# Kernel tuning notes

Measured on AMD Instinct MI355X. Metric: run time of the kernel, lower is better.

Reference implementation:

```python
import jax, jax.numpy as jnp
import numpy as np

D_MODEL = 2048
NUM_EXPERTS = 64
TOP_K = 2


def setup_inputs() -> dict:
    key = jax.random.key(0)
    k_x, k_w = jax.random.split(key)
    x = jax.random.normal(k_x, (4, 8192, D_MODEL), dtype=jnp.float32)
    # nn.Linear(d_model, num_experts, bias=False): weight [num_experts, d_model]
    bound = 1.0 / np.sqrt(D_MODEL)
    W = jax.random.uniform(k_w, (NUM_EXPERTS, D_MODEL), dtype=jnp.float32,
                           minval=-bound, maxval=bound)
    return {"x": x, "W": W}


def reference(x, W):
    # router_logits = x @ W.T : [b, s, num_experts]
    logits = jnp.einsum("bsd,ed->bse", x, W)
    probs = jax.nn.softmax(logits, axis=-1)
    gates, indices = jax.lax.top_k(probs, TOP_K)  # [b, s, top_k]
    gates = gates / jnp.sum(gates, axis=-1, keepdims=True)
    return gates, indices
```

## Files before the change

### kernel.cpp

```cpp
#include <hip/hip_runtime.h>
#include <math.h>
#include <stdint.h>

#define D_MODEL 2048
#define NEXP    64
#define TOKENS  32768
#define BM      64
#define BK      64
#define NT      256
#define NCHUNK  (D_MODEL / BK)
#define TIE_THR 1e-3f
#define LSTRIDE 66

typedef __attribute__((ext_vector_type(8))) short short8;
typedef __attribute__((ext_vector_type(4))) float f32x4;
typedef __attribute__((ext_vector_type(4))) int   i32x4;

typedef __attribute__((address_space(3))) uint32_t       lds_u32_t;
typedef const __attribute__((address_space(1))) uint32_t gbl_u32_t;

#define STAGE(c, b)                                                            \
    _Pragma("unroll")                                                          \
    for (int g = 0; g < 4; ++g) {                                              \
        const int G_ = 4 * wave + g;                                           \
        __builtin_amdgcn_global_load_lds((gbl_u32_t*)(xsrc[g] + (size_t)(c) * BK), \
                                         (lds_u32_t*)&xs[b][4 * G_][0], 16, 0, 0); \
        __builtin_amdgcn_global_load_lds((gbl_u32_t*)(wsrc[g] + (size_t)(c) * BK), \
                                         (lds_u32_t*)&ws[b][4 * G_][0], 16, 0, 0); \
    }

__device__ __forceinline__ void split2(float f0, float f1, uint32_t& hw, uint32_t& lw)
{
    const uint32_t u0 = __float_as_uint(f0), u1 = __float_as_uint(f1);
    const uint32_t a0 = u0 & 0xffff0000u,  a1 = u1 & 0xffff0000u;
    hw = a1 | (u0 >> 16);
    const float l0 = f0 - __uint_as_float(a0);
    const float l1 = f1 - __uint_as_float(a1);
    lw = (__float_as_uint(l1) & 0xffff0000u) | (__float_as_uint(l0) >> 16);
}

__device__ __forceinline__ void ldsplit(const char* p0, const char* p1,
                                        short8& h8, short8& l8)
{
    const float4 qa = *(const float4*)p0;
    const float4 qb = *(const float4*)p1;
    i32x4 hv, lv;
    uint32_t hw, lw;
    split2(qa.x, qa.y, hw, lw); hv[0] = (int)hw; lv[0] = (int)lw;
    split2(qa.z, qa.w, hw, lw); hv[1] = (int)hw; lv[1] = (int)lw;
    split2(qb.x, qb.y, hw, lw); hv[2] = (int)hw; lv[2] = (int)lw;
    split2(qb.z, qb.w, hw, lw); hv[3] = (int)hw; lv[3] = (int)lw;
    h8 = *(short8*)&hv;
    l8 = *(short8*)&lv;
}

__global__ __launch_bounds__(NT, 2)
void router_kernel(const float* __restrict__ x, const float* __restrict__ W,
                   float* __restrict__ out)
{
    __shared__ float xs[2][BM][BK];
    __shared__ float ws[2][NEXP][BK];
    __shared__ int   flaglist[BM];
    __shared__ int   nflag;

    const int tid  = threadIdx.x;
    const int lane = tid & 63;
    const int wave = tid >> 6;
    const int row0 = blockIdx.x * BM;

    const int lrow  = lane >> 4;
    const int lslot = lane & 15;
    const float* xsrc[4];
    const float* wsrc[4];
#pragma unroll
    for (int g = 0; g < 4; ++g) {
        const int r   = 16 * wave + 4 * g + lrow;
        const int col = 4 * (lslot ^ (r & 7));
        xsrc[g] = x + (size_t)(row0 + r) * D_MODEL + col;
        wsrc[g] = W + (size_t)r * D_MODEL + col;
    }

    const int fr  = lane & 15;
    const int h   = lane >> 4;
    const int sw  = 16 * (fr & 7);
    const int t0b = (32 * h) ^ sw;
    const int mt0 = 2 * (wave & 1);
    const int nt0 = 2 * (wave >> 1);
    const int rowA[2] = { (16 * (mt0 + 0) + fr) * 256, (16 * (mt0 + 1) + fr) * 256 };
    const int rowB[2] = { (16 * (nt0 + 0) + fr) * 256, (16 * (nt0 + 1) + fr) * 256 };

    f32x4 acc[2][2] = {};

    STAGE(0, 0);
    __syncthreads();

    for (int c = 0; c < NCHUNK; ++c) {
        const int buf = c & 1;
        if (c + 1 < NCHUNK) STAGE(c + 1, buf ^ 1);
        const char* xb = (const char*)&xs[buf][0][0];
        const char* wb = (const char*)&ws[buf][0][0];
#pragma unroll
        for (int s = 0; s < 2; ++s) {
            const int off0 = 128 * s + t0b;
            short8 ah[2], al[2], bh[2], bl[2];
#pragma unroll
            for (int mi = 0; mi < 2; ++mi)
                ldsplit(xb + rowA[mi] + off0, xb + rowA[mi] + (off0 ^ 16), ah[mi], al[mi]);
#pragma unroll
            for (int ni = 0; ni < 2; ++ni)
                ldsplit(wb + rowB[ni] + off0, wb + rowB[ni] + (off0 ^ 16), bh[ni], bl[ni]);
#pragma unroll
            for (int mi = 0; mi < 2; ++mi)
#pragma unroll
                for (int ni = 0; ni < 2; ++ni) {
                    acc[mi][ni] = __builtin_amdgcn_mfma_f32_16x16x32_bf16(ah[mi], bh[ni], acc[mi][ni], 0, 0, 0);
                    acc[mi][ni] = __builtin_amdgcn_mfma_f32_16x16x32_bf16(al[mi], bh[ni], acc[mi][ni], 0, 0, 0);
                    acc[mi][ni] = __builtin_amdgcn_mfma_f32_16x16x32_bf16(ah[mi], bl[ni], acc[mi][ni], 0, 0, 0);
                }
        }
        __syncthreads();
    }

    float* logits = (float*)&xs[0][0][0];
#pragma unroll
    for (int mi = 0; mi < 2; ++mi)
#pragma unroll
        for (int ni = 0; ni < 2; ++ni)
#pragma unroll
            for (int r = 0; r < 4; ++r)
                logits[(16 * (mt0 + mi) + 4 * h + r) * LSTRIDE + 16 * (nt0 + ni) + fr] =
                    acc[mi][ni][r];
    if (tid == 0) nflag = 0;
    __syncthreads();

    float m1 = -INFINITY, m2 = -INFINITY, m3 = -INFINITY;
    int   i1 = 0, i2 = 0;
    bool  tie = false;
    if (tid < BM) {
#pragma unroll 8
        for (int e = 0; e < NEXP; ++e) {
            const float v = logits[tid * LSTRIDE + e];
            if (v > m1)      { m3 = m2; m2 = m1; i2 = i1; m1 = v; i1 = e; }
            else if (v > m2) { m3 = m2; m2 = v; i2 = e; }
            else if (v > m3) { m3 = v; }
        }
        tie = (m1 - m2 < TIE_THR) || (m2 - m3 < TIE_THR);
        if (tie) { const int p = atomicAdd(&nflag, 1); flaglist[p] = tid; }
    }
    __syncthreads();

    const int nf = nflag;
    float* partial = (float*)&ws[0][0][0];
    for (int f = 0; f < nf; ++f) {
        const int t = flaglist[f];
        const float* xr   = x + (size_t)(row0 + t) * D_MODEL + 512 * wave;
        const float* wrow = W + (size_t)lane * D_MODEL + 512 * wave;
        float ps = 0.f;
        for (int k = 0; k < 512; k += 4) {
            const float4 xv = *(const float4*)(xr + k);
            const float4 wv = *(const float4*)(wrow + k);
            ps = fmaf(xv.x, wv.x, ps); ps = fmaf(xv.y, wv.y, ps);
            ps = fmaf(xv.z, wv.z, ps); ps = fmaf(xv.w, wv.w, ps);
        }
        partial[wave * 64 + lane] = ps;
        __syncthreads();
        if (tid < NEXP)
            logits[t * LSTRIDE + tid] = (partial[tid] + partial[64 + tid]) +
                                        (partial[128 + tid] + partial[192 + tid]);
        __syncthreads();
    }

    if (tid < BM) {
        if (tie) {
            m1 = -INFINITY; m2 = -INFINITY; i1 = 0; i2 = 0;
#pragma unroll 8
            for (int e = 0; e < NEXP; ++e) {
                const float v = logits[tid * LSTRIDE + e];
                if (v > m1)      { m2 = m1; i2 = i1; m1 = v; i1 = e; }
                else if (v > m2) { m2 = v; i2 = e; }
            }
        }
        const float ex = expf(m2 - m1);
        const float g1 = 1.0f / (1.0f + ex);
        const float g2 = ex * g1;
        const int row = row0 + tid;
        out[(size_t)row * 2 + 0] = g1;
        out[(size_t)row * 2 + 1] = g2;
        out[(size_t)TOKENS * 2 + (size_t)row * 2 + 0] = (float)i1;
        out[(size_t)TOKENS * 2 + (size_t)row * 2 + 1] = (float)i2;
    }
}

extern "C" void kernel_launch(void* const* d_in, const int* in_sizes, int n_in,
                              void* d_out, int out_size, void* d_ws, size_t ws_size,
                              hipStream_t stream) {
    const float* x = (const float*)d_in[0];
    const float* W = (const float*)d_in[1];
    float* out = (float*)d_out;
    router_kernel<<<TOKENS / BM, NT, 0, stream>>>(x, W, out);
}
```

Before: 179.0 us.

## Use 128-row tiles, 8 waves, and a 4-stage async LDS pipeline

After: 183.6 us. 2.6% more time.

```diff
diff --git a/kernel.cpp b/kernel.cpp
--- a/kernel.cpp
+++ b/kernel.cpp
@@ -5,10 +5,11 @@
 #define D_MODEL 2048
 #define NEXP    64
 #define TOKENS  32768
-#define BM      64
-#define BK      64
-#define NT      256
+#define BM      128
+#define BK      32
+#define NT      512
 #define NCHUNK  (D_MODEL / BK)
+#define BUFSZ   24576
 #define TIE_THR 1e-3f
 #define LSTRIDE 66
 
@@ -19,20 +20,10 @@
 typedef __attribute__((address_space(3))) uint32_t       lds_u32_t;
 typedef const __attribute__((address_space(1))) uint32_t gbl_u32_t;
 
-#define STAGE(c, b)                                                            \
-    _Pragma("unroll")                                                          \
-    for (int g = 0; g < 4; ++g) {                                              \
-        const int G_ = 4 * wave + g;                                           \
-        __builtin_amdgcn_global_load_lds((gbl_u32_t*)(xsrc[g] + (size_t)(c) * BK), \
-                                         (lds_u32_t*)&xs[b][4 * G_][0], 16, 0, 0); \
-        __builtin_amdgcn_global_load_lds((gbl_u32_t*)(wsrc[g] + (size_t)(c) * BK), \
-                                         (lds_u32_t*)&ws[b][4 * G_][0], 16, 0, 0); \
-    }
-
 __device__ __forceinline__ void split2(float f0, float f1, uint32_t& hw, uint32_t& lw)
 {
     const uint32_t u0 = __float_as_uint(f0), u1 = __float_as_uint(f1);
-    const uint32_t a0 = u0 & 0xffff0000u,  a1 = u1 & 0xffff0000u;
+    const uint32_t a0 = u0 & 0xffff0000u, a1 = u1 & 0xffff0000u;
     hw = a1 | (u0 >> 16);
     const float l0 = f0 - __uint_as_float(a0);
     const float l1 = f1 - __uint_as_float(a1);
@@ -54,81 +45,99 @@
     l8 = *(short8*)&lv;
 }
 
+#define WAITVM(N) asm volatile("s_waitcnt vmcnt(" #N ")" ::: "memory")
+
+#define STAGE(c, b)                                                              \
+    do {                                                                         \
+        char* bb_ = smem + (b) * BUFSZ;                                          \
+        __builtin_amdgcn_global_load_lds((gbl_u32_t*)(xsrc0 + (size_t)(c) * BK), \
+            (lds_u32_t*)(bb_ + 2048 * wave), 16, 0, 0);                          \
+        __builtin_amdgcn_global_load_lds((gbl_u32_t*)(xsrc1 + (size_t)(c) * BK), \
+            (lds_u32_t*)(bb_ + 2048 * wave + 1024), 16, 0, 0);                   \
+        __builtin_amdgcn_global_load_lds((gbl_u32_t*)(wsrc0 + (size_t)(c) * BK), \
+            (lds_u32_t*)(bb_ + 16384 + 1024 * wave), 16, 0, 0);                  \
+    } while (0)
+
+#define COMPUTE(b)                                                               \
+    do {                                                                         \
+        const char* xb_ = smem + (b) * BUFSZ;                                    \
+        const char* wb_ = xb_ + 16384;                                           \
+        short8 ah_[2], al_[2], bh_[2], bl_[2];                                   \
+        _Pragma("unroll")                                                        \
+        for (int mi = 0; mi < 2; ++mi)                                           \
+            ldsplit(xb_ + oA[mi], xb_ + (oA[mi] ^ 16), ah_[mi], al_[mi]);        \
+        _Pragma("unroll")                                                        \
+        for (int ni = 0; ni < 2; ++ni)                                           \
+            ldsplit(wb_ + oB[ni], wb_ + (oB[ni] ^ 16), bh_[ni], bl_[ni]);        \
+        _Pragma("unroll")                                                        \
+        for (int mi = 0; mi < 2; ++mi)                                           \
+            _Pragma("unroll")                                                    \
+            for (int ni = 0; ni < 2; ++ni) {                                     \
+                acc[mi][ni] = __builtin_amdgcn_mfma_f32_16x16x32_bf16(ah_[mi], bh_[ni], acc[mi][ni], 0, 0, 0); \
+                acc[mi][ni] = __builtin_amdgcn_mfma_f32_16x16x32_bf16(al_[mi], bh_[ni], acc[mi][ni], 0, 0, 0); \
+                acc[mi][ni] = __builtin_amdgcn_mfma_f32_16x16x32_bf16(ah_[mi], bl_[ni], acc[mi][ni], 0, 0, 0); \
+            }                                                                    \
+    } while (0)
+
 __global__ __launch_bounds__(NT, 2)
 void router_kernel(const float* __restrict__ x, const float* __restrict__ W,
                    float* __restrict__ out)
 {
-    __shared__ float xs[2][BM][BK];
-    __shared__ float ws[2][NEXP][BK];
-    __shared__ int   flaglist[BM];
-    __shared__ int   nflag;
+    __shared__ char smem[4 * BUFSZ];
+    __shared__ int  flaglist[BM];
+    __shared__ int  nflag;
 
     const int tid  = threadIdx.x;
     const int lane = tid & 63;
     const int wave = tid >> 6;
     const int row0 = blockIdx.x * BM;
 
-    const int lrow  = lane >> 4;
-    const int lslot = lane & 15;
-    const float* xsrc[4];
-    const float* wsrc[4];
-#pragma unroll
-    for (int g = 0; g < 4; ++g) {
-        const int r   = 16 * wave + 4 * g + lrow;
-        const int col = 4 * (lslot ^ (r & 7));
-        xsrc[g] = x + (size_t)(row0 + r) * D_MODEL + col;
-        wsrc[g] = W + (size_t)r * D_MODEL + col;
-    }
-
-    const int fr  = lane & 15;
-    const int h   = lane >> 4;
-    const int sw  = 16 * (fr & 7);
-    const int t0b = (32 * h) ^ sw;
-    const int mt0 = 2 * (wave & 1);
-    const int nt0 = 2 * (wave >> 1);
-    const int rowA[2] = { (16 * (mt0 + 0) + fr) * 256, (16 * (mt0 + 1) + fr) * 256 };
-    const int rowB[2] = { (16 * (nt0 + 0) + fr) * 256, (16 * (nt0 + 1) + fr) * 256 };
+    const int srow = lane >> 3;
+    const int scol = 4 * ((lane & 7) ^ srow);
+    const float* xsrc0 = x + (size_t)(row0 + 16 * wave + srow) * D_MODEL + scol;
+    const float* xsrc1 = x + (size_t)(row0 + 16 * wave + 8 + srow) * D_MODEL + scol;
+    const float* wsrc0 = W + (size_t)(8 * wave + srow) * D_MODEL + scol;
+
+    const int fr = lane & 15;
+    const int h  = lane >> 4;
+    const int m0 = 32 * (wave >> 1);
+    const int n0 = 32 * (wave & 1);
+    int oA[2], oB[2];
+#pragma unroll
+    for (int i = 0; i < 2; ++i) {
+        oA[i] = (m0 + 16 * i + fr) * 128 + 16 * ((2 * h) ^ (fr & 7));
+        oB[i] = (n0 + 16 * i + fr) * 128 + 16 * ((2 * h) ^ (fr & 7));
+    }
 
     f32x4 acc[2][2] = {};
 
     STAGE(0, 0);
+    STAGE(1, 1);
+    STAGE(2, 2);
+
+    for (int c = 0; c < NCHUNK - 3; ++c) {
+        WAITVM(6);
+        __builtin_amdgcn_s_barrier();
+        __builtin_amdgcn_sched_barrier(0);
+        STAGE(c + 3, (c + 3) & 3);
+        COMPUTE(c & 3);
+    }
+    WAITVM(6); __builtin_amdgcn_s_barrier(); __builtin_amdgcn_sched_barrier(0);
+    COMPUTE((NCHUNK - 3) & 3);
+    WAITVM(3); __builtin_amdgcn_s_barrier(); __builtin_amdgcn_sched_barrier(0);
+    COMPUTE((NCHUNK - 2) & 3);
+    WAITVM(0); __builtin_amdgcn_s_barrier(); __builtin_amdgcn_sched_barrier(0);
+    COMPUTE((NCHUNK - 1) & 3);
     __syncthreads();
 
-    for (int c = 0; c < NCHUNK; ++c) {
-        const int buf = c & 1;
-        if (c + 1 < NCHUNK) STAGE(c + 1, buf ^ 1);
-        const char* xb = (const char*)&xs[buf][0][0];
-        const char* wb = (const char*)&ws[buf][0][0];
-#pragma unroll
-        for (int s = 0; s < 2; ++s) {
-            const int off0 = 128 * s + t0b;
-            short8 ah[2], al[2], bh[2], bl[2];
-#pragma unroll
-            for (int mi = 0; mi < 2; ++mi)
-                ldsplit(xb + rowA[mi] + off0, xb + rowA[mi] + (off0 ^ 16), ah[mi], al[mi]);
-#pragma unroll
-            for (int ni = 0; ni < 2; ++ni)
-                ldsplit(wb + rowB[ni] + off0, wb + rowB[ni] + (off0 ^ 16), bh[ni], bl[ni]);
-#pragma unroll
-            for (int mi = 0; mi < 2; ++mi)
-#pragma unroll
-                for (int ni = 0; ni < 2; ++ni) {
-                    acc[mi][ni] = __builtin_amdgcn_mfma_f32_16x16x32_bf16(ah[mi], bh[ni], acc[mi][ni], 0, 0, 0);
-                    acc[mi][ni] = __builtin_amdgcn_mfma_f32_16x16x32_bf16(al[mi], bh[ni], acc[mi][ni], 0, 0, 0);
-                    acc[mi][ni] = __builtin_amdgcn_mfma_f32_16x16x32_bf16(ah[mi], bl[ni], acc[mi][ni], 0, 0, 0);
-                }
-        }
-        __syncthreads();
-    }
-
-    float* logits = (float*)&xs[0][0][0];
+    float* logits = (float*)smem;
 #pragma unroll
     for (int mi = 0; mi < 2; ++mi)
 #pragma unroll
         for (int ni = 0; ni < 2; ++ni)
 #pragma unroll
             for (int r = 0; r < 4; ++r)
-                logits[(16 * (mt0 + mi) + 4 * h + r) * LSTRIDE + 16 * (nt0 + ni) + fr] =
+                logits[(m0 + 16 * mi + 4 * h + r) * LSTRIDE + n0 + 16 * ni + fr] =
                     acc[mi][ni][r];
     if (tid == 0) nflag = 0;
     __syncthreads();
@@ -150,13 +159,13 @@
     __syncthreads();
 
     const int nf = nflag;
-    float* partial = (float*)&ws[0][0][0];
+    float* partial = (float*)(smem + 65536);
     for (int f = 0; f < nf; ++f) {
         const int t = flaglist[f];
-        const float* xr   = x + (size_t)(row0 + t) * D_MODEL + 512 * wave;
-        const float* wrow = W + (size_t)lane * D_MODEL + 512 * wave;
+        const float* xr   = x + (size_t)(row0 + t) * D_MODEL + 256 * wave;
+        const float* wrow = W + (size_t)lane * D_MODEL + 256 * wave;
         float ps = 0.f;
-        for (int k = 0; k < 512; k += 4) {
+        for (int k = 0; k < 256; k += 4) {
             const float4 xv = *(const float4*)(xr + k);
             const float4 wv = *(const float4*)(wrow + k);
             ps = fmaf(xv.x, wv.x, ps); ps = fmaf(xv.y, wv.y, ps);
@@ -164,9 +173,12 @@
         }
         partial[wave * 64 + lane] = ps;
         __syncthreads();
-        if (tid < NEXP)
-            logits[t * LSTRIDE + tid] = (partial[tid] + partial[64 + tid]) +
-                                        (partial[128 + tid] + partial[192 + tid]);
+        if (tid < NEXP) {
+            float s = 0.f;
+#pragma unroll
+            for (int wv = 0; wv < 8; ++wv) s += partial[wv * 64 + tid];
+            logits[t * LSTRIDE + tid] = s;
+        }
         __syncthreads();
     }
 
```

## Load GEMM operands directly from global into registers, drop LDS staging

Applied to the files above, without the earlier changes.

Result: slower. 267.5 us (+49.4%).

```diff
diff --git a/kernel.cpp b/kernel.cpp
--- a/kernel.cpp
+++ b/kernel.cpp
@@ -6,9 +6,8 @@
 #define NEXP    64
 #define TOKENS  32768
 #define BM      64
-#define BK      64
 #define NT      256
-#define NCHUNK  (D_MODEL / BK)
+#define NCHUNK  (D_MODEL / 32)
 #define TIE_THR 1e-3f
 #define LSTRIDE 66
 
@@ -16,34 +15,19 @@
 typedef __attribute__((ext_vector_type(4))) float f32x4;
 typedef __attribute__((ext_vector_type(4))) int   i32x4;
 
-typedef __attribute__((address_space(3))) uint32_t       lds_u32_t;
-typedef const __attribute__((address_space(1))) uint32_t gbl_u32_t;
-
-#define STAGE(c, b)                                                            \
-    _Pragma("unroll")                                                          \
-    for (int g = 0; g < 4; ++g) {                                              \
-        const int G_ = 4 * wave + g;                                           \
-        __builtin_amdgcn_global_load_lds((gbl_u32_t*)(xsrc[g] + (size_t)(c) * BK), \
-                                         (lds_u32_t*)&xs[b][4 * G_][0], 16, 0, 0); \
-        __builtin_amdgcn_global_load_lds((gbl_u32_t*)(wsrc[g] + (size_t)(c) * BK), \
-                                         (lds_u32_t*)&ws[b][4 * G_][0], 16, 0, 0); \
-    }
-
 __device__ __forceinline__ void split2(float f0, float f1, uint32_t& hw, uint32_t& lw)
 {
     const uint32_t u0 = __float_as_uint(f0), u1 = __float_as_uint(f1);
-    const uint32_t a0 = u0 & 0xffff0000u,  a1 = u1 & 0xffff0000u;
+    const uint32_t a0 = u0 & 0xffff0000u, a1 = u1 & 0xffff0000u;
     hw = a1 | (u0 >> 16);
     const float l0 = f0 - __uint_as_float(a0);
     const float l1 = f1 - __uint_as_float(a1);
     lw = (__float_as_uint(l1) & 0xffff0000u) | (__float_as_uint(l0) >> 16);
 }
 
-__device__ __forceinline__ void ldsplit(const char* p0, const char* p1,
-                                        short8& h8, short8& l8)
+__device__ __forceinline__ void regsplit(const float4 qa, const float4 qb,
+                                         short8& h8, short8& l8)
 {
-    const float4 qa = *(const float4*)p0;
-    const float4 qb = *(const float4*)p1;
     i32x4 hv, lv;
     uint32_t hw, lw;
     split2(qa.x, qa.y, hw, lw); hv[0] = (int)hw; lv[0] = (int)lw;
@@ -54,12 +38,32 @@
     l8 = *(short8*)&lv;
 }
 
+#define ASTEP(c, CA0, CA1, NA0, NA1, DOPREF)                                   \
+    do {                                                                       \
+        if (DOPREF) {                                                          \
+            NA0 = *(const float4*)(xrow + 32 * ((c) + 1));                     \
+            NA1 = *(const float4*)(xrow + 32 * ((c) + 1) + 4);                 \
+        }                                                                      \
+        short8 ah_, al_;                                                       \
+        regsplit(CA0, CA1, ah_, al_);                                          \
+        _Pragma("unroll")                                                      \
+        for (int n = 0; n < 4; ++n) {                                          \
+            const float4 qb0 = *(const float4*)(wrow[n] + 32 * (c));           \
+            const float4 qb1 = *(const float4*)(wrow[n] + 32 * (c) + 4);       \
+            short8 bh_, bl_;                                                   \
+            regsplit(qb0, qb1, bh_, bl_);                                      \
+            acc[n] = __builtin_amdgcn_mfma_f32_16x16x32_bf16(ah_, bh_, acc[n], 0, 0, 0); \
+            acc[n] = __builtin_amdgcn_mfma_f32_16x16x32_bf16(al_, bh_, acc[n], 0, 0, 0); \
+            acc[n] = __builtin_amdgcn_mfma_f32_16x16x32_bf16(ah_, bl_, acc[n], 0, 0, 0); \
+        }                                                                      \
+    } while (0)
+
 __global__ __launch_bounds__(NT, 2)
 void router_kernel(const float* __restrict__ x, const float* __restrict__ W,
                    float* __restrict__ out)
 {
-    __shared__ float xs[2][BM][BK];
-    __shared__ float ws[2][NEXP][BK];
+    __shared__ float logits[BM * LSTRIDE];
+    __shared__ float partial[4 * 64];
     __shared__ int   flaglist[BM];
     __shared__ int   nflag;
 
@@ -68,68 +72,30 @@
     const int wave = tid >> 6;
     const int row0 = blockIdx.x * BM;
 
-    const int lrow  = lane >> 4;
-    const int lslot = lane & 15;
-    const float* xsrc[4];
-    const float* wsrc[4];
+    const int fr = lane & 15;
+    const int h  = lane >> 4;
+    const float* xrow = x + (size_t)(row0 + 16 * wave + fr) * D_MODEL + 8 * h;
+    const float* wrow[4];
 #pragma unroll
-    for (int g = 0; g < 4; ++g) {
-        const int r   = 16 * wave + 4 * g + lrow;
-        const int col = 4 * (lslot ^ (r & 7));
-        xsrc[g] = x + (size_t)(row0 + r) * D_MODEL + col;
-        wsrc[g] = W + (size_t)r * D_MODEL + col;
+    for (int n = 0; n < 4; ++n)
+        wrow[n] = W + (size_t)(16 * n + fr) * D_MODEL + 8 * h;
+
+    f32x4 acc[4] = {};
+
+    float4 pa0, pa1, qa0, qa1;
+    pa0 = *(const float4*)(xrow);
+    pa1 = *(const float4*)(xrow + 4);
+#pragma unroll 1
+    for (int cc = 0; cc < NCHUNK / 2; ++cc) {
+        ASTEP(2 * cc,     pa0, pa1, qa0, qa1, 1);
+        ASTEP(2 * cc + 1, qa0, qa1, pa0, pa1, (cc < NCHUNK / 2 - 1));
     }
 
-    const int fr  = lane & 15;
-    const int h   = lane >> 4;
-    const int sw  = 16 * (fr & 7);
-    const int t0b = (32 * h) ^ sw;
-    const int mt0 = 2 * (wave & 1);
-    const int nt0 = 2 * (wave >> 1);
-    const int rowA[2] = { (16 * (mt0 + 0) + fr) * 256, (16 * (mt0 + 1) + fr) * 256 };
-    const int rowB[2] = { (16 * (nt0 + 0) + fr) * 256, (16 * (nt0 + 1) + fr) * 256 };
-
-    f32x4 acc[2][2] = {};
-
-    STAGE(0, 0);
-    __syncthreads();
-
-    for (int c = 0; c < NCHUNK; ++c) {
-        const int buf = c & 1;
-        if (c + 1 < NCHUNK) STAGE(c + 1, buf ^ 1);
-        const char* xb = (const char*)&xs[buf][0][0];
-        const char* wb = (const char*)&ws[buf][0][0];
 #pragma unroll
-        for (int s = 0; s < 2; ++s) {
-            const int off0 = 128 * s + t0b;
-            short8 ah[2], al[2], bh[2], bl[2];
+    for (int n = 0; n < 4; ++n)
 #pragma unroll
-            for (int mi = 0; mi < 2; ++mi)
-                ldsplit(xb + rowA[mi] + off0, xb + rowA[mi] + (off0 ^ 16), ah[mi], al[mi]);
-#pragma unroll
-            for (int ni = 0; ni < 2; ++ni)
-                ldsplit(wb + rowB[ni] + off0, wb + rowB[ni] + (off0 ^ 16), bh[ni], bl[ni]);
-#pragma unroll
-            for (int mi = 0; mi < 2; ++mi)
-#pragma unroll
-                for (int ni = 0; ni < 2; ++ni) {
-                    acc[mi][ni] = __builtin_amdgcn_mfma_f32_16x16x32_bf16(ah[mi], bh[ni], acc[mi][ni], 0, 0, 0);
-                    acc[mi][ni] = __builtin_amdgcn_mfma_f32_16x16x32_bf16(al[mi], bh[ni], acc[mi][ni], 0, 0, 0);
-                    acc[mi][ni] = __builtin_amdgcn_mfma_f32_16x16x32_bf16(ah[mi], bl[ni], acc[mi][ni], 0, 0, 0);
-                }
-        }
-        __syncthreads();
-    }
-
-    float* logits = (float*)&xs[0][0][0];
-#pragma unroll
-    for (int mi = 0; mi < 2; ++mi)
-#pragma unroll
-        for (int ni = 0; ni < 2; ++ni)
-#pragma unroll
-            for (int r = 0; r < 4; ++r)
-                logits[(16 * (mt0 + mi) + 4 * h + r) * LSTRIDE + 16 * (nt0 + ni) + fr] =
-                    acc[mi][ni][r];
+        for (int r = 0; r < 4; ++r)
+            logits[(16 * wave + 4 * h + r) * LSTRIDE + 16 * n + fr] = acc[n][r];
     if (tid == 0) nflag = 0;
     __syncthreads();
 
@@ -150,15 +116,14 @@
     __syncthreads();
 
     const int nf = nflag;
-    float* partial = (float*)&ws[0][0][0];
     for (int f = 0; f < nf; ++f) {
         const int t = flaglist[f];
         const float* xr   = x + (size_t)(row0 + t) * D_MODEL + 512 * wave;
-        const float* wrow = W + (size_t)lane * D_MODEL + 512 * wave;
+        const float* wrw  = W + (size_t)lane * D_MODEL + 512 * wave;
         float ps = 0.f;
         for (int k = 0; k < 512; k += 4) {
             const float4 xv = *(const float4*)(xr + k);
-            const float4 wv = *(const float4*)(wrow + k);
+            const float4 wv = *(const float4*)(wrw + k);
             ps = fmaf(xv.x, wv.x, ps); ps = fmaf(xv.y, wv.y, ps);
             ps = fmaf(xv.z, wv.z, ps); ps = fmaf(xv.w, wv.w, ps);
         }
```
